# Optimization experiments

Measured on AMD Instinct MI355X. Metric: run time of the kernel, lower is better.

## Reference

```python
import jax, jax.numpy as jnp
import numpy as np

N_NODES = 256
N_SECRETS = 64
N_INPUTS = 16      # per-node source-node inputs
N_SECDEP = 8       # per-node secret-dependency columns
ENTRIES = 3 + N_INPUTS + N_SECDEP  # 27
ACTION_SIZE = 4096
BATCH = 8192
STATE_DIM = N_NODES + N_SECRETS + 2  # 322


def _build_index_matrix() -> np.ndarray:
    """idx[i] = column indices of `state` concatenated for node i, mirroring split()."""
    rng = np.random.default_rng(1234)
    idx = np.empty((N_NODES, ENTRIES), dtype=np.int32)
    g0 = N_NODES + N_SECRETS  # first of the two global columns
    for i in range(N_NODES):
        src = rng.integers(0, N_NODES, size=N_INPUTS)           # inputs[j].sourceNodeIndex
        sec = N_NODES + rng.choice(N_SECRETS, size=N_SECDEP, replace=False)  # secrIndex[i]
        idx[i] = np.concatenate(([i, g0, g0 + 1], src, np.sort(sec)))
    return idx


def setup_inputs() -> dict:
    key = jax.random.key(0)
    k1, k2, k3, k4 = jax.random.split(key, 4)
    state = jax.random.normal(k1, (BATCH, STATE_DIM), dtype=jnp.float32)
    # per-node Linear(ENTRIES, 1): weight [N, E], bias [N]
    bound = 1.0 / np.sqrt(ENTRIES)
    W = jax.random.uniform(k2, (N_NODES, ENTRIES), jnp.float32, -bound, bound)
    b = jax.random.uniform(k3, (N_NODES,), jnp.float32, -bound, bound)
    # final Linear(N_NODES, ACTION_SIZE, bias=False): weight [A, N]
    bf = 1.0 / np.sqrt(N_NODES)
    Wf = jax.random.uniform(k4, (ACTION_SIZE, N_NODES), jnp.float32, -bf, bf)
    idx = jnp.asarray(_build_index_matrix())
    return {"state": state, "W": W, "b": b, "Wf": Wf, "idx": idx}


def reference(state, W, b, Wf, idx):
    # split(): per-node gather of ENTRIES columns -> [B, N, E]
    gathered = jnp.take(state, idx, axis=1)
    # per-node tiny Linear + tanh -> [B, N]
    y = jnp.tanh(jnp.einsum("bne,ne->bn", gathered, W) + b)
    # final linear (no bias), scaled sigmoid -> [B, A]
    return 500.0 * jax.nn.sigmoid(jnp.einsum("bn,an->ba", y, Wf))
```

## Files before the change

### kernel.cpp

```cpp
#include <hip/hip_runtime.h>
#include <hip/hip_bf16.h>
#include <cmath>

#define ENTRIES 27
#define ACTION  4096
#define BATCH   8192
#define SDIM    322
#define KPAD    352
#define NNODES  256

typedef unsigned short u16;
typedef u16 u16x4 __attribute__((ext_vector_type(4)));
typedef u16 u16x8 __attribute__((ext_vector_type(8)));
typedef __bf16 bf16x8 __attribute__((ext_vector_type(8)));
typedef float floatx4 __attribute__((ext_vector_type(4)));

__device__ __forceinline__ u16 f2bf(float f) {
    unsigned u = __builtin_bit_cast(unsigned, f);
    unsigned r = (u + 0x7FFFu + ((u >> 16) & 1u)) >> 16;
    return (u16)r;
}

__device__ __forceinline__ float sig500(float v) {
    return __fdividef(500.0f, 1.0f + __expf(-v));
}
__device__ __forceinline__ float ftanh(float x) {
    return 1.0f - __fdividef(2.0f, __expf(2.0f * x) + 1.0f);
}

__device__ __forceinline__ void gl_lds16(const u16* g, u16* l) {
    __builtin_amdgcn_global_load_lds(
        (const __attribute__((address_space(1))) unsigned int*)g,
        (__attribute__((address_space(3))) unsigned int*)l, 16, 0, 0);
}

#define PREP_WF0   32
#define PREP_ST0   1056
#define PREP_TOT   3872

__global__ __launch_bounds__(256) void prep_kernel(
    const float* __restrict__ W, const int* __restrict__ idx,
    const float* __restrict__ wf, const float* __restrict__ state,
    u16* __restrict__ wg, u16* __restrict__ wfb, u16* __restrict__ sbf)
{
    const int tid = threadIdx.x;
    const int bid = blockIdx.x;

    if (bid < PREP_WF0) {
        __shared__ float rows[8 * KPAD];
        for (int i = tid; i < 8 * KPAD; i += 256) rows[i] = 0.f;
        __syncthreads();
        if (tid < 8 * ENTRIES) {
            const int nl = tid / ENTRIES;
            const int e  = tid - nl * ENTRIES;
            const int n  = bid * 8 + nl;
            atomicAdd(&rows[nl * KPAD + idx[n * ENTRIES + e]],
                      W[n * ENTRIES + e]);
        }
        __syncthreads();
        for (int i = tid; i < 8 * KPAD; i += 256)
            wg[(size_t)bid * 8 * KPAD + i] = f2bf(rows[i]);
    } else if (bid < PREP_ST0) {
        const int i0 = ((bid - PREP_WF0) * 256 + tid) * 4;
        floatx4 v = *(const floatx4*)(wf + i0);
        u16x4 r;
        r.x = f2bf(v.x); r.y = f2bf(v.y); r.z = f2bf(v.z); r.w = f2bf(v.w);
        *(u16x4*)(wfb + i0) = r;
    } else {
        const int t   = (bid - PREP_ST0) * 256 + tid;
        const int row = t / 88;
        const int c0  = (t - row * 88) * 4;
        const float* sp = state + (size_t)row * SDIM;
        u16x4 r;
#pragma unroll
        for (int q = 0; q < 4; q++) {
            const int c = c0 + q;
            float v = (c < SDIM) ? sp[c] : 0.f;
            ((u16*)&r)[q] = f2bf(v);
        }
        *(u16x4*)(sbf + (size_t)row * KPAD + c0) = r;
    }
}

template<int KDIM, int EPI, int BN>
__global__ __launch_bounds__(256) void gemm_mfma(
    const u16* __restrict__ A, const u16* __restrict__ B,
    void* __restrict__ outp, const float* __restrict__ bias)
{
    constexpr int NI  = BN / 32;
    constexpr int WN  = BN / 2;
    constexpr int ACH = 8;
    constexpr int BCH = BN / 16;

    __shared__ u16 As[128 * 32];
    __shared__ u16 Bs[BN * 32];

    const int bm   = blockIdx.x;
    const int bn   = blockIdx.y;
    const int tid  = threadIdx.x;
    const int lane = tid & 63;
    const int wave = tid >> 6;
    const int wm   = wave & 1;
    const int wn   = wave >> 1;
    const int l15  = lane & 15;
    const int koff = (lane >> 4) << 3;

    floatx4 acc[4][NI];
#pragma unroll
    for (int mi = 0; mi < 4; mi++)
#pragma unroll
        for (int ni = 0; ni < NI; ni++)
            acc[mi][ni] = (floatx4){0.f, 0.f, 0.f, 0.f};

    const int crow = lane >> 2;
    const int ckel = (lane & 3) << 3;

#pragma unroll
    for (int kk = 0; kk < KDIM; kk += 32) {
        __syncthreads();
#pragma unroll
        for (int c = wave; c < ACH + BCH; c += 4) {
            const bool isA = c < ACH;
            const int  cr  = isA ? c : c - ACH;
            const int  row = cr * 16 + crow;
            const u16* g = isA
                ? (A + ((size_t)bm * 128 + row) * KDIM + kk + ckel)
                : (B + ((size_t)bn * BN  + row) * KDIM + kk + ckel);
            u16* l = isA ? &As[cr * 512] : &Bs[cr * 512];
            gl_lds16(g, l);
        }
        __syncthreads();

        bf16x8 af[4], bfg[NI];
#pragma unroll
        for (int mi = 0; mi < 4; mi++)
            af[mi] = __builtin_bit_cast(bf16x8,
                *(const u16x8*)&As[((wm << 6) + (mi << 4) + l15) * 32 + koff]);
#pragma unroll
        for (int ni = 0; ni < NI; ni++)
            bfg[ni] = __builtin_bit_cast(bf16x8,
                *(const u16x8*)&Bs[(wn * WN + (ni << 4) + l15) * 32 + koff]);

#pragma unroll
        for (int mi = 0; mi < 4; mi++)
#pragma unroll
            for (int ni = 0; ni < NI; ni++)
                acc[mi][ni] = __builtin_amdgcn_mfma_f32_16x16x32_bf16(
                    af[mi], bfg[ni], acc[mi][ni], 0, 0, 0);
    }

    const int r0 = (lane >> 4) << 2;
    float bv[NI];
    if (EPI == 1) {
#pragma unroll
        for (int ni = 0; ni < NI; ni++)
            bv[ni] = bias[bn * BN + wn * WN + ni * 16 + l15];
    }
#pragma unroll
    for (int mi = 0; mi < 4; mi++) {
#pragma unroll
        for (int ni = 0; ni < NI; ni++) {
            const int row = bm * 128 + wm * 64 + mi * 16 + r0;
            const int col = bn * BN + wn * WN + ni * 16 + l15;
#pragma unroll
            for (int r = 0; r < 4; r++) {
                float v = acc[mi][ni][r];
                if (EPI == 0) {
                    ((float*)outp)[(size_t)(row + r) * ACTION + col] = sig500(v);
                } else {
                    ((u16*)outp)[(size_t)(row + r) * NNODES + col] =
                        f2bf(ftanh(v + bv[ni]));
                }
            }
        }
    }
}

extern "C" void kernel_launch(void* const* d_in, const int* in_sizes, int n_in,
                              void* d_out, int out_size, void* d_ws, size_t ws_size,
                              hipStream_t stream) {
    const float* state = (const float*)d_in[0];
    const float* W     = (const float*)d_in[1];
    const float* b     = (const float*)d_in[2];
    const float* Wf    = (const float*)d_in[3];
    const int*   idx   = (const int*)  d_in[4];
    float* out = (float*)d_out;

    u16* sbf = (u16*)d_ws;
    u16* wg  = sbf + (size_t)BATCH * KPAD;
    u16* y   = wg  + (size_t)NNODES * KPAD;
    u16* wfb = y   + (size_t)BATCH * NNODES;

    prep_kernel<<<PREP_TOT, 256, 0, stream>>>(W, idx, Wf, state, wg, wfb, sbf);
    gemm_mfma<KPAD, 1, 64><<<dim3(BATCH / 128, NNODES / 64), 256, 0, stream>>>(
        sbf, wg, (void*)y, b);
    gemm_mfma<256, 0, 128><<<dim3(BATCH / 128, ACTION / 128), 256, 0, stream>>>(
        y, wfb, (void*)out, nullptr);
}
```

Baseline: 176.8 us.

## Fuse state fp32-to-bf16 conversion into first GEMM with resident weight tile

Removes the separate pass that converted the state matrix to a padded bf16 workspace, and instead loads fp32 state directly inside a new first-stage GEMM kernel, converting in registers before staging to LDS. The whole 64xKPAD weight slice is loaded once into LDS per block, and A tiles are software-prefetched one k-step ahead. This is meant to cut the extra global write and reread of the bf16 state copy, at the cost of smaller 64x64 tiles, uncoalesced-ish 8-float row loads and extra syncs per k-step.

Measured after the change: 176.6 us. No clear change (-0.1%).

```diff
diff --git a/kernel.cpp b/kernel.cpp
--- a/kernel.cpp
+++ b/kernel.cpp
@@ -1,5 +1,4 @@
 #include <hip/hip_runtime.h>
-#include <hip/hip_bf16.h>
 #include <cmath>
 
 #define ENTRIES 27
@@ -13,6 +12,7 @@
 typedef u16 u16x4 __attribute__((ext_vector_type(4)));
 typedef u16 u16x8 __attribute__((ext_vector_type(8)));
 typedef __bf16 bf16x8 __attribute__((ext_vector_type(8)));
+typedef float floatx2 __attribute__((ext_vector_type(2)));
 typedef float floatx4 __attribute__((ext_vector_type(4)));
 
 __device__ __forceinline__ u16 f2bf(float f) {
@@ -20,28 +20,25 @@
     unsigned r = (u + 0x7FFFu + ((u >> 16) & 1u)) >> 16;
     return (u16)r;
 }
-
 __device__ __forceinline__ float sig500(float v) {
     return __fdividef(500.0f, 1.0f + __expf(-v));
 }
 __device__ __forceinline__ float ftanh(float x) {
     return 1.0f - __fdividef(2.0f, __expf(2.0f * x) + 1.0f);
 }
-
 __device__ __forceinline__ void gl_lds16(const u16* g, u16* l) {
     __builtin_amdgcn_global_load_lds(
         (const __attribute__((address_space(1))) unsigned int*)g,
         (__attribute__((address_space(3))) unsigned int*)l, 16, 0, 0);
 }
 
-#define PREP_WF0   32
-#define PREP_ST0   1056
-#define PREP_TOT   3872
+#define PREP_WF0 32
+#define PREP_TOT 1056
 
 __global__ __launch_bounds__(256) void prep_kernel(
     const float* __restrict__ W, const int* __restrict__ idx,
-    const float* __restrict__ wf, const float* __restrict__ state,
-    u16* __restrict__ wg, u16* __restrict__ wfb, u16* __restrict__ sbf)
+    const float* __restrict__ wf,
+    u16* __restrict__ wg, u16* __restrict__ wfb)
 {
     const int tid = threadIdx.x;
     const int bid = blockIdx.x;
@@ -60,26 +57,109 @@
         __syncthreads();
         for (int i = tid; i < 8 * KPAD; i += 256)
             wg[(size_t)bid * 8 * KPAD + i] = f2bf(rows[i]);
-    } else if (bid < PREP_ST0) {
+    } else {
         const int i0 = ((bid - PREP_WF0) * 256 + tid) * 4;
         floatx4 v = *(const floatx4*)(wf + i0);
         u16x4 r;
         r.x = f2bf(v.x); r.y = f2bf(v.y); r.z = f2bf(v.z); r.w = f2bf(v.w);
         *(u16x4*)(wfb + i0) = r;
-    } else {
-        const int t   = (bid - PREP_ST0) * 256 + tid;
-        const int row = t / 88;
-        const int c0  = (t - row * 88) * 4;
-        const float* sp = state + (size_t)row * SDIM;
-        u16x4 r;
-#pragma unroll
-        for (int q = 0; q < 4; q++) {
-            const int c = c0 + q;
-            float v = (c < SDIM) ? sp[c] : 0.f;
-            ((u16*)&r)[q] = f2bf(v);
-        }
-        *(u16x4*)(sbf + (size_t)row * KPAD + c0) = r;
-    }
+    }
+}
+
+__global__ __launch_bounds__(256) void gemm1_fused(
+    const float* __restrict__ state, const u16* __restrict__ wg,
+    u16* __restrict__ y, const float* __restrict__ bias)
+{
+    __shared__ u16 Bs[64 * KPAD];
+    __shared__ u16 As[64 * 32];
+
+    const int bm   = blockIdx.x;
+    const int bn   = blockIdx.y;
+    const int tid  = threadIdx.x;
+    const int lane = tid & 63;
+    const int wave = tid >> 6;
+    const int wm   = wave & 1;
+    const int wn   = wave >> 1;
+    const int l15  = lane & 15;
+    const int koff = (lane >> 4) << 3;
+
+    const u16* wgp = wg + (size_t)bn * 64 * KPAD;
+    for (int c = wave; c < 44; c += 4)
+        gl_lds16(wgp + c * 512 + lane * 8, &Bs[c * 512]);
+
+    const int arow = tid >> 2;
+    const int qseg = tid & 3;
+    const float* ap = state + (size_t)(bm * 64 + arow) * SDIM + qseg * 8;
+    float va[8];
+
+    auto loada = [&](int kk) {
+        const int c0 = kk + qseg * 8;
+        const float* p = ap + kk;
+        if (c0 + 8 <= SDIM) {
+#pragma unroll
+            for (int j = 0; j < 4; j++)
+                *(floatx2*)&va[2 * j] = *(const floatx2*)(p + 2 * j);
+        } else {
+#pragma unroll
+            for (int j = 0; j < 8; j++)
+                va[j] = (c0 + j < SDIM) ? p[j] : 0.f;
+        }
+    };
+    loada(0);
+
+    floatx4 acc[2][2];
+#pragma unroll
+    for (int mi = 0; mi < 2; mi++)
+#pragma unroll
+        for (int ni = 0; ni < 2; ni++)
+            acc[mi][ni] = (floatx4){0.f, 0.f, 0.f, 0.f};
+
+#pragma unroll
+    for (int s = 0; s < 11; s++) {
+        const int kk = s * 32;
+        u16x8 pk;
+#pragma unroll
+        for (int j = 0; j < 8; j++) ((u16*)&pk)[j] = f2bf(va[j]);
+
+        __syncthreads();
+        *(u16x8*)&As[arow * 32 + qseg * 8] = pk;
+        __syncthreads();
+
+        if (s < 10) loada(kk + 32);
+
+        bf16x8 af[2], bfr[2];
+#pragma unroll
+        for (int mi = 0; mi < 2; mi++)
+            af[mi] = __builtin_bit_cast(bf16x8,
+                *(const u16x8*)&As[((wm << 5) + (mi << 4) + l15) * 32 + koff]);
+#pragma unroll
+        for (int ni = 0; ni < 2; ni++)
+            bfr[ni] = __builtin_bit_cast(bf16x8,
+                *(const u16x8*)&Bs[(wn * 32 + ni * 16 + l15) * KPAD + kk + koff]);
+#pragma unroll
+        for (int mi = 0; mi < 2; mi++)
+#pragma unroll
+            for (int ni = 0; ni < 2; ni++)
+                acc[mi][ni] = __builtin_amdgcn_mfma_f32_16x16x32_bf16(
+                    af[mi], bfr[ni], acc[mi][ni], 0, 0, 0);
+    }
+
+    const int r0 = (lane >> 4) << 2;
+    float bv[2];
+#pragma unroll
+    for (int ni = 0; ni < 2; ni++)
+        bv[ni] = bias[bn * 64 + wn * 32 + ni * 16 + l15];
+#pragma unroll
+    for (int mi = 0; mi < 2; mi++)
+#pragma unroll
+        for (int ni = 0; ni < 2; ni++) {
+            const int row = bm * 64 + wm * 32 + mi * 16 + r0;
+            const int col = bn * 64 + wn * 32 + ni * 16 + l15;
+#pragma unroll
+            for (int r = 0; r < 4; r++)
+                y[(size_t)(row + r) * NNODES + col] =
+                    f2bf(ftanh(acc[mi][ni][r] + bv[ni]));
+        }
 }
 
 template<int KDIM, int EPI, int BN>
@@ -186,14 +266,12 @@
     const int*   idx   = (const int*)  d_in[4];
     float* out = (float*)d_out;
 
-    u16* sbf = (u16*)d_ws;
-    u16* wg  = sbf + (size_t)BATCH * KPAD;
-    u16* y   = wg  + (size_t)NNODES * KPAD;
-    u16* wfb = y   + (size_t)BATCH * NNODES;
-
-    prep_kernel<<<PREP_TOT, 256, 0, stream>>>(W, idx, Wf, state, wg, wfb, sbf);
-    gemm_mfma<KPAD, 1, 64><<<dim3(BATCH / 128, NNODES / 64), 256, 0, stream>>>(
-        sbf, wg, (void*)y, b);
+    u16* wg  = (u16*)d_ws;
+    u16* y   = wg + (size_t)NNODES * KPAD;
+    u16* wfb = y  + (size_t)BATCH * NNODES;
+
+    prep_kernel<<<PREP_TOT, 256, 0, stream>>>(W, idx, Wf, wg, wfb);
+    gemm1_fused<<<dim3(128, 4), 256, 0, stream>>>(state, wg, y, b);
     gemm_mfma<256, 0, 128><<<dim3(BATCH / 128, ACTION / 128), 256, 0, stream>>>(
         y, wfb, (void*)out, nullptr);
 }
```
